# Performance work log

Measured on AMD Instinct MI355X. Metric: run time of the kernel, lower is better.

Reference implementation:

```python
import jax, jax.numpy as jnp
import numpy as np

N_FEAT = 350; D = 512; L = 4; DS = 64; NREG = 6; REG_E = 32
B = 32; S = 2048
CLAMP = 20.0


def _ln(x, g, b, eps=1e-5):
    mu = jnp.mean(x, axis=-1, keepdims=True)
    var = jnp.mean(jnp.square(x - mu), axis=-1, keepdims=True)
    return (x - mu) * jax.lax.rsqrt(var + eps) * g + b


def _slstm(x, ln_g, ln_b, Wi, bi, Wf, bf, Wz, bz, Wo, bo, Wp, bp):
    # x: [B,S,D] -> out: [B,S,D]
    xn = _ln(x, ln_g, ln_b)
    log_i = jnp.clip(jnp.einsum('bsd,de->bse', xn, Wi) + bi, -CLAMP, CLAMP)
    log_f = jnp.clip(jnp.einsum('bsd,de->bse', xn, Wf) + bf, -CLAMP, CLAMP)
    z = jnp.tanh(jnp.einsum('bsd,de->bse', xn, Wz) + bz)
    o = jax.nn.sigmoid(jnp.einsum('bsd,de->bse', xn, Wo) + bo)

    def step(carry, inp):
        m, c = carry
        li, lf, zt, ot = inp
        m_new = jnp.maximum(m + lf, li)
        i_s = jnp.exp(li - m_new)
        f_s = jnp.exp(m + lf - m_new)
        c_new = f_s * c + i_s * zt
        h = ot * jnp.tanh(c_new)
        return (m_new, c_new), h

    bsz = x.shape[0]
    init = (jnp.zeros((bsz, DS), x.dtype), jnp.zeros((bsz, DS), x.dtype))
    seq = (jnp.swapaxes(log_i, 0, 1), jnp.swapaxes(log_f, 0, 1),
           jnp.swapaxes(z, 0, 1), jnp.swapaxes(o, 0, 1))
    _, hs = jax.lax.scan(step, init, seq)  # hs: [S,B,DS]
    hs = jnp.swapaxes(hs, 0, 1)  # [B,S,DS]
    return jnp.einsum('bse,ed->bsd', hs, Wp) + bp


def setup_inputs() -> dict:
    key = jax.random.key(0)
    ks = iter(jax.random.split(key, 64))
    def p(*shape):
        return jax.random.normal(next(ks), shape, dtype=jnp.float32) * 0.02
    return {
        'x': jax.random.normal(next(ks), (B, S, N_FEAT), dtype=jnp.float32),
        'regime_ids': jax.random.randint(next(ks), (B, S), 0, NREG),
        'emb_regime': p(NREG, REG_E),
        'grn_w1': p(N_FEAT + REG_E, D), 'grn_b1': jnp.zeros((D,), jnp.float32),
        'grn_w2': p(D, N_FEAT), 'grn_b2': jnp.zeros((N_FEAT,), jnp.float32),
        'in_w': p(N_FEAT, D), 'in_b': jnp.zeros((D,), jnp.float32),
        'ln_in_g': jnp.ones((L, D), jnp.float32), 'ln_in_b': jnp.zeros((L, D), jnp.float32),
        'wi': p(L, D, DS), 'bi': jnp.zeros((L, DS), jnp.float32),
        'wf': p(L, D, DS), 'bf': jnp.zeros((L, DS), jnp.float32),
        'wz': p(L, D, DS), 'bz': jnp.zeros((L, DS), jnp.float32),
        'wo': p(L, D, DS), 'bo': jnp.zeros((L, DS), jnp.float32),
        'wp': p(L, DS, D), 'bp': jnp.zeros((L, D), jnp.float32),
        'nm_g': jnp.ones((L, D), jnp.float32), 'nm_b': jnp.zeros((L, D), jnp.float32),
        'hd15_w': p(D, 1), 'hd15_b': jnp.zeros((1,), jnp.float32),
        'hd30_w': p(D, 1), 'hd30_b': jnp.zeros((1,), jnp.float32),
        'hv_w': p(D, 3), 'hv_b': jnp.zeros((3,), jnp.float32),
        'hreg_w': p(D, NREG), 'hreg_b': jnp.zeros((NREG,), jnp.float32),
        'hrng_w': p(D, 3), 'hrng_b': jnp.zeros((3,), jnp.float32),
    }


def reference(x, regime_ids, emb_regime, grn_w1, grn_b1, grn_w2, grn_b2,
              in_w, in_b, ln_in_g, ln_in_b, wi, bi, wf, bf, wz, bz, wo, bo,
              wp, bp, nm_g, nm_b, hd15_w, hd15_b, hd30_w, hd30_b,
              hv_w, hv_b, hreg_w, hreg_b, hrng_w, hrng_b):
    # Variable selection network (regime-conditioned feature weights)
    remb = emb_regime[regime_ids]                      # [B,S,32]
    comb = jnp.concatenate([x, remb], axis=-1)         # [B,S,382]
    hidden = jax.nn.elu(jnp.einsum('bsf,fd->bsd', comb, grn_w1) + grn_b1)
    weights = jax.nn.softmax(jnp.einsum('bsd,df->bsf', hidden, grn_w2) + grn_b2, axis=-1)
    xw = x * weights
    h = jnp.einsum('bsf,fd->bsd', xw, in_w) + in_b     # [B,S,D]
    for l in range(L):
        res = _slstm(h, ln_in_g[l], ln_in_b[l], wi[l], bi[l], wf[l], bf[l],
                     wz[l], bz[l], wo[l], bo[l], wp[l], bp[l])
        h = _ln(h + res, nm_g[l], nm_b[l])
    h_last = h[:, -1, :]
    return (jnp.squeeze(h_last @ hd15_w + hd15_b, -1),
            jnp.squeeze(h_last @ hd30_w + hd30_b, -1),
            h_last @ hv_w + hv_b,
            h_last @ hreg_w + hreg_b,
            h_last @ hrng_w + hrng_b,
            h_last,
            weights[:, -1, :])
```

## Files before the change

### kernel.cpp

```cpp
#include <hip/hip_runtime.h>
#include <cmath>

#define NFEAT 350
#define DMODEL 512
#define NLAYER 4
#define DSZ 64
#define REG_E 32
#define BATCH 32
#define SEQ 2048
#define MTOK (BATCH * SEQ)
#define CLAMP_V 20.0f

#define CHUNK 64
#define NCHUNK (SEQ / CHUNK)

typedef short bf16x8 __attribute__((ext_vector_type(8)));
typedef float f32x4 __attribute__((ext_vector_type(4)));

__device__ __forceinline__ unsigned short f2b(float v) {
    union { float f; unsigned int u; } x; x.f = v;
    unsigned int r = x.u + 0x7fffu + ((x.u >> 16) & 1u);
    return (unsigned short)(r >> 16);
}
__device__ __forceinline__ float b2f(unsigned short u) {
    union { unsigned int i; float f; } x; x.i = ((unsigned int)u) << 16;
    return x.f;
}
__device__ __forceinline__ unsigned int pack2(float a, float b) {
    return ((unsigned int)f2b(b) << 16) | f2b(a);
}

__global__ __launch_bounds__(256) void tconv_k(const float* __restrict__ src,
                                               unsigned short* __restrict__ dst,
                                               int K, int N, int Kpad) {
    int k = blockIdx.x * 256 + threadIdx.x;
    int n = blockIdx.y;
    if (k >= Kpad) return;
    float v = (k < K && n < N) ? src[(size_t)k * N + n] : 0.f;
    dst[(size_t)n * Kpad + k] = f2b(v);
}

__global__ __launch_bounds__(256) void tconv_wp_k(const float* __restrict__ wp,
                                                  unsigned short* __restrict__ dst) {
    int idx = blockIdx.x * 256 + threadIdx.x;
    int l = idx >> 15;
    int rem = idx & 32767;
    int n = rem >> 6;
    int k = rem & 63;
    float v = wp[((size_t)l * 64 + k) * 512 + n];
    unsigned short hi = f2b(v);
    unsigned short lo = f2b(v - b2f(hi));
    unsigned short* d = dst + ((size_t)l * 512 + n) * 128;
    d[k] = hi;
    d[64 + k] = lo;
}

__global__ __launch_bounds__(256) void tconv_g_k(const float* __restrict__ wi,
                                                 const float* __restrict__ wf,
                                                 const float* __restrict__ wz,
                                                 const float* __restrict__ wo,
                                                 unsigned short* __restrict__ dst) {
    int k = blockIdx.x * 256 + threadIdx.x;
    int n = blockIdx.y;
    int z = blockIdx.z;
    int l = z >> 2, g = z & 3;
    const float* src = (g == 0 ? wi : g == 1 ? wf : g == 2 ? wz : wo) + (size_t)l * DMODEL * DSZ;
    dst[(size_t)z * 32768 + (size_t)n * 512 + k] = f2b(src[(size_t)k * DSZ + n]);
}

__global__ __launch_bounds__(1024) void gbias_k(const float* bi, const float* bf_,
                                                const float* bz, const float* bo,
                                                float* __restrict__ gbias) {
    int t = threadIdx.x;
    int l = t >> 8, r = t & 255, g = r >> 6, e = r & 63;
    const float* s = (g == 0 ? bi : g == 1 ? bf_ : g == 2 ? bz : bo);
    gbias[t] = s[l * 64 + e];
}

__global__ __launch_bounds__(256) void build_xc_k(const float* __restrict__ x,
                                                  const int* __restrict__ rid,
                                                  const float* __restrict__ emb,
                                                  unsigned short* __restrict__ xc) {
    int i = blockIdx.x * 256 + threadIdx.x;
    int m = i / 192, p = i - m * 192;
    int k = p * 2;
    float a = 0.f, b = 0.f;
    if (k < 350) {
        const float2 v = *(const float2*)(x + (size_t)m * NFEAT + k);
        a = v.x; b = v.y;
    } else if (k < 382) {
        int r = rid[m];
        const float2 v = *(const float2*)(emb + r * REG_E + (k - 350));
        a = v.x; b = v.y;
    }
    ((unsigned int*)xc)[(size_t)m * 192 + p] = pack2(a, b);
}

template <int ALD, int EPI>
__global__ __launch_bounds__(256) void mgemm_k(const unsigned short* __restrict__ Ab,
                                               const float* __restrict__ Af,
                                               const unsigned short* __restrict__ Bt,
                                               const float* __restrict__ bias,
                                               float* __restrict__ Cf,
                                               unsigned short* __restrict__ Cb,
                                               const float* __restrict__ muA,
                                               const float* __restrict__ rstdA,
                                               const float* __restrict__ lng,
                                               const float* __restrict__ lnb,
                                               int lda, int ldb, int K, int N, int ldc) {
    __shared__ unsigned short As[128][40];
    __shared__ unsigned short Bs[128][40];
    const int tid = threadIdx.x;
    const int lane = tid & 63;
    const int wave = tid >> 6;
    const int l15 = lane & 15;
    const int quad = lane >> 4;
    const int wm = (wave >> 1) * 64;
    const int wn = (wave & 1) * 64;
    const size_t m0 = (size_t)blockIdx.y * 128;
    const int n0 = blockIdx.x * 128;

    const int sr = tid >> 2;
    const int ku = tid & 3;

    const unsigned short* Br0 = Bt + ((size_t)(n0 + sr)) * ldb + ku * 8;
    const unsigned short* Br1 = Br0 + (size_t)64 * ldb;

    const unsigned short* Ar0 = nullptr;
    const unsigned short* Ar1 = nullptr;
    const float* Fr0 = nullptr;
    const float* Fr1 = nullptr;
    float mu0 = 0.f, rs0 = 0.f, mu1 = 0.f, rs1 = 0.f;
    if (ALD == 0) {
        Ar0 = Ab + (m0 + sr) * (size_t)lda + ku * 8;
        Ar1 = Ar0 + (size_t)64 * lda;
    } else {
        Fr0 = Af + (m0 + sr) * (size_t)lda + ku * 8;
        Fr1 = Fr0 + (size_t)64 * lda;
        mu0 = muA[m0 + sr];   rs0 = rstdA[m0 + sr];
        mu1 = muA[m0 + sr + 64]; rs1 = rstdA[m0 + sr + 64];
    }

    f32x4 acc[4][4] = {};

    for (int k0 = 0; k0 < K; k0 += 32) {
        if (ALD == 0) {
            *(uint4*)&As[sr][ku * 8]      = *(const uint4*)(Ar0 + k0);
            *(uint4*)&As[sr + 64][ku * 8] = *(const uint4*)(Ar1 + k0);
        } else {
            float4 g0 = *(const float4*)(lng + k0 + ku * 8);
            float4 g1 = *(const float4*)(lng + k0 + ku * 8 + 4);
            float4 c0 = *(const float4*)(lnb + k0 + ku * 8);
            float4 c1 = *(const float4*)(lnb + k0 + ku * 8 + 4);
            {
                float4 v0 = *(const float4*)(Fr0 + k0);
                float4 v1 = *(const float4*)(Fr0 + k0 + 4);
                uint4 w;
                w.x = pack2((v0.x - mu0) * rs0 * g0.x + c0.x, (v0.y - mu0) * rs0 * g0.y + c0.y);
                w.y = pack2((v0.z - mu0) * rs0 * g0.z + c0.z, (v0.w - mu0) * rs0 * g0.w + c0.w);
                w.z = pack2((v1.x - mu0) * rs0 * g1.x + c1.x, (v1.y - mu0) * rs0 * g1.y + c1.y);
                w.w = pack2((v1.z - mu0) * rs0 * g1.z + c1.z, (v1.w - mu0) * rs0 * g1.w + c1.w);
                *(uint4*)&As[sr][ku * 8] = w;
            }
            {
                float4 v0 = *(const float4*)(Fr1 + k0);
                float4 v1 = *(const float4*)(Fr1 + k0 + 4);
                uint4 w;
                w.x = pack2((v0.x - mu1) * rs1 * g0.x + c0.x, (v0.y - mu1) * rs1 * g0.y + c0.y);
                w.y = pack2((v0.z - mu1) * rs1 * g0.z + c0.z, (v0.w - mu1) * rs1 * g0.w + c0.w);
                w.z = pack2((v1.x - mu1) * rs1 * g1.x + c1.x, (v1.y - mu1) * rs1 * g1.y + c1.y);
                w.w = pack2((v1.z - mu1) * rs1 * g1.z + c1.z, (v1.w - mu1) * rs1 * g1.w + c1.w);
                *(uint4*)&As[sr + 64][ku * 8] = w;
            }
        }
        *(uint4*)&Bs[sr][ku * 8]      = *(const uint4*)(Br0 + k0);
        *(uint4*)&Bs[sr + 64][ku * 8] = *(const uint4*)(Br1 + k0);
        __syncthreads();
        bf16x8 af[4], bf[4];
#pragma unroll
        for (int mt = 0; mt < 4; mt++)
            af[mt] = *(const bf16x8*)&As[wm + mt * 16 + l15][quad * 8];
#pragma unroll
        for (int nt = 0; nt < 4; nt++)
            bf[nt] = *(const bf16x8*)&Bs[wn + nt * 16 + l15][quad * 8];
#pragma unroll
        for (int mt = 0; mt < 4; mt++)
#pragma unroll
            for (int nt = 0; nt < 4; nt++)
                acc[mt][nt] = __builtin_amdgcn_mfma_f32_16x16x32_bf16(af[mt], bf[nt], acc[mt][nt], 0, 0, 0);
        __syncthreads();
    }

#pragma unroll
    for (int mt = 0; mt < 4; mt++) {
        int gmb = wm + mt * 16 + quad * 4;
#pragma unroll
        for (int nt = 0; nt < 4; nt++) {
            int gn = n0 + wn + nt * 16 + l15;
            if (gn < N) {
                float bv = bias[gn];
#pragma unroll
                for (int r = 0; r < 4; r++) {
                    size_t gm = m0 + gmb + r;
                    float v = acc[mt][nt][r] + bv;
                    if (EPI == 0) {
                        v = v > 0.f ? v : expm1f(v);
                        Cb[gm * (size_t)ldc + gn] = f2b(v);
                    } else if (EPI == 1) {
                        Cb[gm * (size_t)ldc + gn] = f2b(v);
                    } else if (EPI == 2) {
                        int g = gn >> 6;
                        if (g < 2) v = fminf(fmaxf(v, -CLAMP_V), CLAMP_V);
                        else if (g == 2) v = tanhf(v);
                        else v = 1.f / (1.f + expf(-v));
                        Cf[gm * (size_t)ldc + gn] = v;
                    } else {
                        Cf[gm * (size_t)ldc + gn] = v;
                    }
                }
            }
        }
    }
}

__global__ __launch_bounds__(256) void softmax_xw_k(const unsigned short* __restrict__ logits,
                                                    unsigned short* __restrict__ xc,
                                                    float* __restrict__ out_wlast) {
    int tok = blockIdx.x * 4 + (threadIdx.x >> 6);
    int lane = threadIdx.x & 63;
    const unsigned short* lr = logits + (size_t)tok * NFEAT;
    unsigned short* xr = xc + (size_t)tok * 384;
    float v[6];
    float mx = -1e30f;
#pragma unroll
    for (int i = 0; i < 6; i++) {
        int idx = lane + 64 * i;
        v[i] = (idx < NFEAT) ? b2f(lr[idx]) : -1e30f;
        mx = fmaxf(mx, v[i]);
    }
#pragma unroll
    for (int o = 32; o > 0; o >>= 1) mx = fmaxf(mx, __shfl_xor(mx, o, 64));
    float s = 0.f;
#pragma unroll
    for (int i = 0; i < 6; i++) { v[i] = expf(v[i] - mx); s += v[i]; }
#pragma unroll
    for (int o = 32; o > 0; o >>= 1) s += __shfl_xor(s, o, 64);
    float inv = 1.f / s;
    bool last = ((tok & (SEQ - 1)) == SEQ - 1);
    int b = tok >> 11;
#pragma unroll
    for (int i = 0; i < 6; i++) {
        int idx = lane + 64 * i;
        if (idx < NFEAT) {
            float w = v[i] * inv;
            xr[idx] = f2b(w * b2f(xr[idx]));
            if (last) out_wlast[b * NFEAT + idx] = w;
        } else if (idx < 352) {
            xr[idx] = 0;
        }
    }
}

__global__ __launch_bounds__(256) void ln_stats_k(const float* __restrict__ h,
                                                  float* __restrict__ mu,
                                                  float* __restrict__ rstd) {
    int tok = blockIdx.x * 4 + (threadIdx.x >> 6);
    int lane = threadIdx.x & 63;
    const float* row = h + (size_t)tok * DMODEL;
    float s = 0.f, sq = 0.f;
#pragma unroll
    for (int i = 0; i < 8; i++) {
        float v = row[lane + 64 * i];
        s += v;
        sq += v * v;
    }
#pragma unroll
    for (int o = 32; o > 0; o >>= 1) {
        s += __shfl_xor(s, o, 64);
        sq += __shfl_xor(sq, o, 64);
    }
    if (lane == 0) {
        float m = s * (1.f / DMODEL);
        float var = sq * (1.f / DMODEL) - m * m;
        mu[tok] = m;
        rstd[tok] = rsqrtf(var + 1e-5f);
    }
}

__global__ __launch_bounds__(256) void seg_agg_k(const float* __restrict__ gates,
                                                 float* __restrict__ aggF,
                                                 float* __restrict__ aggL,
                                                 float* __restrict__ aggS) {
    int b = blockIdx.x >> 3;
    int cg = blockIdx.x & 7;
    int chunk = cg * 4 + (threadIdx.x >> 6);
    int e = threadIdx.x & 63;
    const float* gp = gates + ((size_t)b * SEQ + (size_t)chunk * CHUNK) * 256;
    float F = 0.f, L = -1e30f, s = 0.f;
#pragma unroll 4
    for (int t = 0; t < CHUNK; t++) {
        const float* q = gp + (size_t)t * 256;
        float li = q[e], lf = q[64 + e], z = q[128 + e];
        float Ln = fmaxf(L + lf, li);
        s = expf(L + lf - Ln) * s + expf(li - Ln) * z;
        L = Ln;
        F += lf;
    }
    int idx = (b * NCHUNK + chunk) * 64 + e;
    aggF[idx] = F; aggL[idx] = L; aggS[idx] = s;
}

__global__ __launch_bounds__(64) void chunk_scan_k(const float* __restrict__ aggF,
                                                   const float* __restrict__ aggL,
                                                   const float* __restrict__ aggS,
                                                   float* __restrict__ stM,
                                                   float* __restrict__ stC) {
    int b = blockIdx.x;
    int e = threadIdx.x;
    float m = 0.f, c = 0.f;
    for (int k = 0; k < NCHUNK; k++) {
        int idx = (b * NCHUNK + k) * 64 + e;
        stM[idx] = m; stC[idx] = c;
        float F = aggF[idx], L = aggL[idx], s = aggS[idx];
        float mn = fmaxf(m + F, L);
        c = expf(m + F - mn) * c + expf(L - mn) * s;
        m = mn;
    }
}

__global__ __launch_bounds__(256) void replay_k(const float* __restrict__ gates,
                                                const float* __restrict__ stM,
                                                const float* __restrict__ stC,
                                                unsigned short* __restrict__ hs) {
    int b = blockIdx.x >> 3;
    int cg = blockIdx.x & 7;
    int chunk = cg * 4 + (threadIdx.x >> 6);
    int e = threadIdx.x & 63;
    int s0 = chunk * CHUNK;
    const float* gp = gates + ((size_t)b * SEQ + s0) * 256;
    unsigned short* hp = hs + ((size_t)b * SEQ + s0) * 128;
    int idx = (b * NCHUNK + chunk) * 64 + e;
    float m = stM[idx], c = stC[idx];
#pragma unroll 4
    for (int t = 0; t < CHUNK; t++) {
        const float* q = gp + (size_t)t * 256;
        float li = q[e], lf = q[64 + e], z = q[128 + e], o = q[192 + e];
        float mlf = m + lf;
        float mn = fmaxf(mlf, li);
        c = expf(mlf - mn) * c + expf(li - mn) * z;
        m = mn;
        float v = o * tanhf(c);
        unsigned short hi = f2b(v);
        hp[(size_t)t * 128 + e] = hi;
        hp[(size_t)t * 128 + 64 + e] = f2b(v - b2f(hi));
    }
}

__global__ __launch_bounds__(256) void outproj_mfma_k(const unsigned short* __restrict__ hs,
                                                      const unsigned short* __restrict__ wpt,
                                                      const float* __restrict__ bp,
                                                      const float* __restrict__ nmg,
                                                      const float* __restrict__ nmb,
                                                      float* __restrict__ h,
                                                      float* __restrict__ mu,
                                                      float* __restrict__ rstd) {
    __shared__ unsigned short As[16][168];
    __shared__ float proj[16][520];
    const int tid = threadIdx.x;
    const int lane = tid & 63;
    const int wv = tid >> 6;
    const int l15 = lane & 15;
    const int quad = lane >> 4;
    const int wn = wv * 128;
    const size_t tok0 = (size_t)blockIdx.x * 16;

    float bpv[8], gv[8], bv_[8];
#pragma unroll
    for (int j = 0; j < 8; j++) {
        int col = lane + 64 * j;
        bpv[j] = bp[col]; gv[j] = nmg[col]; bv_[j] = nmb[col];
    }

    {
        int row = tid >> 4, ku = tid & 15;
        *(uint4*)&As[row][ku * 8] = *(const uint4*)(hs + (tok0 + row) * 128 + ku * 8);
    }
    __syncthreads();

    bf16x8 a_hi0 = *(const bf16x8*)&As[l15][quad * 8];
    bf16x8 a_hi1 = *(const bf16x8*)&As[l15][32 + quad * 8];
    bf16x8 a_lo0 = *(const bf16x8*)&As[l15][64 + quad * 8];
    bf16x8 a_lo1 = *(const bf16x8*)&As[l15][96 + quad * 8];

    f32x4 acc[8] = {};
#pragma unroll 1
    for (int term = 0; term < 3; term++) {
        const bf16x8 af0 = (term == 2) ? a_lo0 : a_hi0;
        const bf16x8 af1 = (term == 2) ? a_lo1 : a_hi1;
        const int boff = (term == 1) ? 64 : 0;
        bf16x8 bv[2][8];
#pragma unroll
        for (int ks = 0; ks < 2; ks++)
#pragma unroll
            for (int nt = 0; nt < 8; nt++)
                bv[ks][nt] = *(const bf16x8*)(wpt + (size_t)(wn + nt * 16 + l15) * 128 + boff + ks * 32 + quad * 8);
#pragma unroll
        for (int nt = 0; nt < 8; nt++)
            acc[nt] = __builtin_amdgcn_mfma_f32_16x16x32_bf16(af0, bv[0][nt], acc[nt], 0, 0, 0);
#pragma unroll
        for (int nt = 0; nt < 8; nt++)
            acc[nt] = __builtin_amdgcn_mfma_f32_16x16x32_bf16(af1, bv[1][nt], acc[nt], 0, 0, 0);
    }

    float hv[4][8];
#pragma unroll
    for (int t = 0; t < 4; t++)
#pragma unroll
        for (int j = 0; j < 8; j++)
            hv[t][j] = h[(tok0 + wv * 4 + t) * (size_t)DMODEL + lane + 64 * j];

#pragma unroll
    for (int nt = 0; nt < 8; nt++)
#pragma unroll
        for (int r = 0; r < 4; r++)
            proj[quad * 4 + r][wn + nt * 16 + l15] = acc[nt][r];
    __syncthreads();

#pragma unroll
    for (int t = 0; t < 4; t++) {
        int trow = wv * 4 + t;
        size_t tok = tok0 + trow;
        float u[8];
        float s = 0.f, sq = 0.f;
#pragma unroll
        for (int j = 0; j < 8; j++) {
            float v = hv[t][j] + proj[trow][lane + 64 * j] + bpv[j];
            u[j] = v;
            s += v; sq += v * v;
        }
#pragma unroll
        for (int o = 32; o > 0; o >>= 1) { s += __shfl_xor(s, o, 64); sq += __shfl_xor(sq, o, 64); }
        float mean = s * (1.f / DMODEL);
        float var = sq * (1.f / DMODEL) - mean * mean;
        float rs = rsqrtf(var + 1e-5f);
        float* hrow = h + tok * (size_t)DMODEL;
        float s2 = 0.f, sq2 = 0.f;
#pragma unroll
        for (int j = 0; j < 8; j++) {
            float v = (u[j] - mean) * rs * gv[j] + bv_[j];
            hrow[lane + 64 * j] = v;
            s2 += v; sq2 += v * v;
        }
#pragma unroll
        for (int o = 32; o > 0; o >>= 1) { s2 += __shfl_xor(s2, o, 64); sq2 += __shfl_xor(sq2, o, 64); }
        if (lane == 0) {
            float m2 = s2 * (1.f / DMODEL);
            float v2 = sq2 * (1.f / DMODEL) - m2 * m2;
            mu[tok] = m2;
            rstd[tok] = rsqrtf(v2 + 1e-5f);
        }
    }
}

__global__ __launch_bounds__(64) void heads_k(const float* __restrict__ h,
                                              const float* hd15_w, const float* hd15_b,
                                              const float* hd30_w, const float* hd30_b,
                                              const float* hv_w, const float* hv_b,
                                              const float* hreg_w, const float* hreg_b,
                                              const float* hrng_w, const float* hrng_b,
                                              float* __restrict__ out) {
    int b = blockIdx.x;
    int lane = threadIdx.x;
    __shared__ float row[DMODEL];
    const float* hp = h + (size_t)(b * SEQ + SEQ - 1) * DMODEL;
#pragma unroll
    for (int i = 0; i < 8; i++) row[lane + 64 * i] = hp[lane + 64 * i];
    __syncthreads();
#pragma unroll
    for (int i = 0; i < 8; i++) out[448 + b * DMODEL + lane + 64 * i] = row[lane + 64 * i];
    if (lane < 14) {
        const float* w; const float* bb;
        int ncol, j, off;
        if (lane == 0)      { w = hd15_w; bb = hd15_b; ncol = 1; j = 0;         off = 0 + b; }
        else if (lane == 1) { w = hd30_w; bb = hd30_b; ncol = 1; j = 0;         off = 32 + b; }
        else if (lane < 5)  { j = lane - 2;  w = hv_w;   bb = hv_b;   ncol = 3; off = 64 + b * 3 + j; }
        else if (lane < 11) { j = lane - 5;  w = hreg_w; bb = hreg_b; ncol = 6; off = 160 + b * 6 + j; }
        else                { j = lane - 11; w = hrng_w; bb = hrng_b; ncol = 3; off = 352 + b * 3 + j; }
        float s = bb[j];
        for (int k = 0; k < DMODEL; k++) s += row[k] * w[k * ncol + j];
        out[off] = s;
    }
}

extern "C" void kernel_launch(void* const* d_in, const int* in_sizes, int n_in,
                              void* d_out, int out_size, void* d_ws, size_t ws_size,
                              hipStream_t stream) {
    (void)in_sizes; (void)n_in; (void)out_size; (void)ws_size;
    const float* x      = (const float*)d_in[0];
    const int*   rid    = (const int*)d_in[1];
    const float* emb    = (const float*)d_in[2];
    const float* grn_w1 = (const float*)d_in[3];
    const float* grn_b1 = (const float*)d_in[4];
    const float* grn_w2 = (const float*)d_in[5];
    const float* grn_b2 = (const float*)d_in[6];
    const float* in_w   = (const float*)d_in[7];
    const float* in_b   = (const float*)d_in[8];
    const float* ln_g   = (const float*)d_in[9];
    const float* ln_b   = (const float*)d_in[10];
    const float* wi     = (const float*)d_in[11];
    const float* bi     = (const float*)d_in[12];
    const float* wf     = (const float*)d_in[13];
    const float* bf_    = (const float*)d_in[14];
    const float* wz     = (const float*)d_in[15];
    const float* bz     = (const float*)d_in[16];
    const float* wo     = (const float*)d_in[17];
    const float* bo     = (const float*)d_in[18];
    const float* wp     = (const float*)d_in[19];
    const float* bp     = (const float*)d_in[20];
    const float* nm_g   = (const float*)d_in[21];
    const float* nm_b   = (const float*)d_in[22];

    float* out = (float*)d_out;
    char* W = (char*)d_ws;

    float* h               = (float*)W;
    unsigned short* hidden = (unsigned short*)W;
    unsigned short* logits = (unsigned short*)(W + 67108864);
    char* RB = W + 134217728;
    unsigned short* xc = (unsigned short*)RB;
    float* gates  = (float*)RB;
    unsigned short* hsbuf = (unsigned short*)(RB + 67108864);
    char* RM = W + 218103808;
    float* aggF  = (float*)(RM);
    float* aggL  = (float*)(RM + 262144);
    float* aggS  = (float*)(RM + 524288);
    float* stM   = (float*)(RM + 786432);
    float* stC   = (float*)(RM + 1048576);
    float* mu    = (float*)(RM + 1310720);
    float* rstd  = (float*)(RM + 1572864);
    unsigned short* w1t  = (unsigned short*)(RM + 1835008);
    unsigned short* w2t  = (unsigned short*)(RM + 2228224);
    unsigned short* inwt = (unsigned short*)(RM + 2621440);
    unsigned short* gwt  = (unsigned short*)(RM + 2981888);
    float* gbias         = (float*)(RM + 4030464);
    unsigned short* wpt  = (unsigned short*)(RM + 4034560);

    build_xc_k<<<MTOK * 192 / 256, 256, 0, stream>>>(x, rid, emb, xc);
    tconv_k<<<dim3(2, 512), 256, 0, stream>>>(grn_w1, w1t, 382, 512, 384);
    tconv_k<<<dim3(2, 384), 256, 0, stream>>>(grn_w2, w2t, 512, 350, 512);
    tconv_k<<<dim3(2, 512), 256, 0, stream>>>(in_w, inwt, 350, 512, 352);
    tconv_g_k<<<dim3(2, 64, 16), 256, 0, stream>>>(wi, wf, wz, wo, gwt);
    gbias_k<<<1, 1024, 0, stream>>>(bi, bf_, bz, bo, gbias);
    tconv_wp_k<<<512, 256, 0, stream>>>(wp, wpt);

    mgemm_k<0, 0><<<dim3(4, 512), 256, 0, stream>>>(xc, nullptr, w1t, grn_b1, nullptr, hidden,
                                                    nullptr, nullptr, nullptr, nullptr,
                                                    384, 384, 384, 512, 512);
    mgemm_k<0, 1><<<dim3(3, 512), 256, 0, stream>>>(hidden, nullptr, w2t, grn_b2, nullptr, logits,
                                                    nullptr, nullptr, nullptr, nullptr,
                                                    512, 512, 512, 350, 350);
    softmax_xw_k<<<MTOK / 4, 256, 0, stream>>>(logits, xc, out + 16832);
    mgemm_k<0, 3><<<dim3(4, 512), 256, 0, stream>>>(xc, nullptr, inwt, in_b, h, nullptr,
                                                    nullptr, nullptr, nullptr, nullptr,
                                                    384, 352, 352, 512, 512);
    ln_stats_k<<<MTOK / 4, 256, 0, stream>>>(h, mu, rstd);

    for (int l = 0; l < NLAYER; l++) {
        mgemm_k<1, 2><<<dim3(2, 512), 256, 0, stream>>>(nullptr, h, gwt + (size_t)l * 131072,
                                                        gbias + l * 256, gates, nullptr,
                                                        mu, rstd,
                                                        ln_g + l * DMODEL, ln_b + l * DMODEL,
                                                        512, 512, 512, 256, 256);
        seg_agg_k<<<BATCH * 8, 256, 0, stream>>>(gates, aggF, aggL, aggS);
        chunk_scan_k<<<BATCH, 64, 0, stream>>>(aggF, aggL, aggS, stM, stC);
        replay_k<<<BATCH * 8, 256, 0, stream>>>(gates, stM, stC, hsbuf);

        outproj_mfma_k<<<MTOK / 16, 256, 0, stream>>>(hsbuf,
                                                      wpt + (size_t)l * 65536,
                                                      bp + l * DMODEL,
                                                      nm_g + l * DMODEL,
                                                      nm_b + l * DMODEL,
                                                      h, mu, rstd);
    }

    heads_k<<<BATCH, 64, 0, stream>>>(h,
                                      (const float*)d_in[23], (const float*)d_in[24],
                                      (const float*)d_in[25], (const float*)d_in[26],
                                      (const float*)d_in[27], (const float*)d_in[28],
                                      (const float*)d_in[29], (const float*)d_in[30],
                                      (const float*)d_in[31], (const float*)d_in[32],
                                      out);
}
```

Before: 1.415 ms.

## Split outproj across eight waves with aliased shared memory buffers

Measured after the change: 1.391 ms. Within noise of the previous version (-1.7%).

```diff
diff --git a/kernel.cpp b/kernel.cpp
--- a/kernel.cpp
+++ b/kernel.cpp
@@ -356,7 +356,7 @@
     }
 }
 
-__global__ __launch_bounds__(256) void outproj_mfma_k(const unsigned short* __restrict__ hs,
+__global__ __launch_bounds__(512) void outproj_mfma_k(const unsigned short* __restrict__ hs,
                                                       const unsigned short* __restrict__ wpt,
                                                       const float* __restrict__ bp,
                                                       const float* __restrict__ nmg,
@@ -364,26 +364,20 @@
                                                       float* __restrict__ h,
                                                       float* __restrict__ mu,
                                                       float* __restrict__ rstd) {
-    __shared__ unsigned short As[16][168];
-    __shared__ float proj[16][520];
+    __shared__ __attribute__((aligned(16))) char smem[33024];
+    unsigned short (*As)[168] = (unsigned short (*)[168])smem;
+    float (*proj)[516] = (float (*)[516])smem;
     const int tid = threadIdx.x;
     const int lane = tid & 63;
     const int wv = tid >> 6;
     const int l15 = lane & 15;
     const int quad = lane >> 4;
-    const int wn = wv * 128;
+    const int wn = wv * 64;
     const size_t tok0 = (size_t)blockIdx.x * 16;
 
-    float bpv[8], gv[8], bv_[8];
-#pragma unroll
-    for (int j = 0; j < 8; j++) {
-        int col = lane + 64 * j;
-        bpv[j] = bp[col]; gv[j] = nmg[col]; bv_[j] = nmb[col];
-    }
-
     {
-        int row = tid >> 4, ku = tid & 15;
-        *(uint4*)&As[row][ku * 8] = *(const uint4*)(hs + (tok0 + row) * 128 + ku * 8);
+        int row = tid >> 5, ku = tid & 31;
+        *(uint2*)&As[row][ku * 4] = *(const uint2*)(hs + (tok0 + row) * 128 + ku * 4);
     }
     __syncthreads();
 
@@ -391,44 +385,53 @@
     bf16x8 a_hi1 = *(const bf16x8*)&As[l15][32 + quad * 8];
     bf16x8 a_lo0 = *(const bf16x8*)&As[l15][64 + quad * 8];
     bf16x8 a_lo1 = *(const bf16x8*)&As[l15][96 + quad * 8];
-
-    f32x4 acc[8] = {};
+    __syncthreads();
+
+    f32x4 acc[4] = {};
+    const unsigned short* wb = wpt + (size_t)(wn + l15) * 128 + quad * 8;
 #pragma unroll 1
     for (int term = 0; term < 3; term++) {
         const bf16x8 af0 = (term == 2) ? a_lo0 : a_hi0;
         const bf16x8 af1 = (term == 2) ? a_lo1 : a_hi1;
         const int boff = (term == 1) ? 64 : 0;
-        bf16x8 bv[2][8];
-#pragma unroll
-        for (int ks = 0; ks < 2; ks++)
-#pragma unroll
-            for (int nt = 0; nt < 8; nt++)
-                bv[ks][nt] = *(const bf16x8*)(wpt + (size_t)(wn + nt * 16 + l15) * 128 + boff + ks * 32 + quad * 8);
-#pragma unroll
-        for (int nt = 0; nt < 8; nt++)
-            acc[nt] = __builtin_amdgcn_mfma_f32_16x16x32_bf16(af0, bv[0][nt], acc[nt], 0, 0, 0);
-#pragma unroll
-        for (int nt = 0; nt < 8; nt++)
-            acc[nt] = __builtin_amdgcn_mfma_f32_16x16x32_bf16(af1, bv[1][nt], acc[nt], 0, 0, 0);
-    }
-
-    float hv[4][8];
-#pragma unroll
-    for (int t = 0; t < 4; t++)
+#pragma unroll
+        for (int ks = 0; ks < 2; ks++) {
+            bf16x8 bv0 = *(const bf16x8*)(wb + 0 * 2048 + boff + ks * 32);
+            bf16x8 bv1 = *(const bf16x8*)(wb + 1 * 2048 + boff + ks * 32);
+            bf16x8 bv2 = *(const bf16x8*)(wb + 2 * 2048 + boff + ks * 32);
+            bf16x8 bv3 = *(const bf16x8*)(wb + 3 * 2048 + boff + ks * 32);
+            const bf16x8 af = ks ? af1 : af0;
+            acc[0] = __builtin_amdgcn_mfma_f32_16x16x32_bf16(af, bv0, acc[0], 0, 0, 0);
+            acc[1] = __builtin_amdgcn_mfma_f32_16x16x32_bf16(af, bv1, acc[1], 0, 0, 0);
+            acc[2] = __builtin_amdgcn_mfma_f32_16x16x32_bf16(af, bv2, acc[2], 0, 0, 0);
+            acc[3] = __builtin_amdgcn_mfma_f32_16x16x32_bf16(af, bv3, acc[3], 0, 0, 0);
+        }
+    }
+
+    float hv[2][8];
+#pragma unroll
+    for (int t = 0; t < 2; t++)
 #pragma unroll
         for (int j = 0; j < 8; j++)
-            hv[t][j] = h[(tok0 + wv * 4 + t) * (size_t)DMODEL + lane + 64 * j];
-
-#pragma unroll
-    for (int nt = 0; nt < 8; nt++)
+            hv[t][j] = h[(tok0 + wv * 2 + t) * (size_t)DMODEL + lane + 64 * j];
+
+#pragma unroll
+    for (int nt = 0; nt < 4; nt++)
 #pragma unroll
         for (int r = 0; r < 4; r++)
             proj[quad * 4 + r][wn + nt * 16 + l15] = acc[nt][r];
     __syncthreads();
 
-#pragma unroll
-    for (int t = 0; t < 4; t++) {
-        int trow = wv * 4 + t;
+    float bpv[8], gv[8], bv_[8];
+#pragma unroll
+    for (int j = 0; j < 8; j++) {
+        int col = lane + 64 * j;
+        bpv[j] = bp[col]; gv[j] = nmg[col]; bv_[j] = nmb[col];
+    }
+
+#pragma unroll
+    for (int t = 0; t < 2; t++) {
+        int trow = wv * 2 + t;
         size_t tok = tok0 + trow;
         float u[8];
         float s = 0.f, sq = 0.f;
@@ -575,7 +578,7 @@
         chunk_scan_k<<<BATCH, 64, 0, stream>>>(aggF, aggL, aggS, stM, stC);
         replay_k<<<BATCH * 8, 256, 0, stream>>>(gates, stM, stC, hsbuf);
 
-        outproj_mfma_k<<<MTOK / 16, 256, 0, stream>>>(hsbuf,
+        outproj_mfma_k<<<MTOK / 16, 512, 0, stream>>>(hsbuf,
                                                       wpt + (size_t)l * 65536,
                                                       bp + l * DMODEL,
                                                       nm_g + l * DMODEL,
```
